# Kernel tuning notes

Hardware: AMD Instinct MI355X
Metric: run time of the kernel (lower is better)

## Reference

```python
import jax, jax.numpy as jnp
import numpy as np

D_MODEL = 1024
NUM_HEADS = 16
HEAD_DIM = D_MODEL // NUM_HEADS


def setup_inputs() -> dict:
    key = jax.random.key(0)
    kx, kq, kk, kv, ko = jax.random.split(key, 5)
    B, T = 2, 2048
    scale = 1.0 / np.sqrt(D_MODEL)
    return {
        "x": jax.random.normal(kx, (B, T, D_MODEL), dtype=jnp.float32),
        "wq": jax.random.normal(kq, (D_MODEL, D_MODEL), dtype=jnp.float32) * scale,
        "wk": jax.random.normal(kk, (D_MODEL, D_MODEL), dtype=jnp.float32) * scale,
        "wv": jax.random.normal(kv, (D_MODEL, D_MODEL), dtype=jnp.float32) * scale,
        "wo": jax.random.normal(ko, (D_MODEL, D_MODEL), dtype=jnp.float32) * scale,
    }


def _split_heads(x):
    b, t, _ = x.shape
    return x.reshape(b, t, NUM_HEADS, HEAD_DIM).transpose(0, 2, 1, 3)  # [b,h,t,d]


def reference(x, wq, wk, wv, wo):
    q = _split_heads(x @ wq)
    k = _split_heads(x @ wk)
    v = _split_heads(x @ wv)
    inv_sqrt_d = jnp.asarray(1.0 / np.sqrt(HEAD_DIM), x.dtype)
    scores = jnp.einsum("bhqd,bhkd->bhqk", q, k) * inv_sqrt_d
    weights = jax.nn.softmax(scores, axis=-1)  # dropout rate 0.0 -> identity
    out = jnp.einsum("bhqk,bhkd->bhqd", weights, v)
    b, h, t, d = out.shape
    out = out.transpose(0, 2, 1, 3).reshape(b, t, D_MODEL)
    return out @ wo
```

## Files before the change

### kernel.cpp

```cpp
#include <hip/hip_runtime.h>
#include <stdint.h>

using bf16   = __bf16;
using bf16x8 = __bf16 __attribute__((ext_vector_type(8)));
using bf16x4 = __bf16 __attribute__((ext_vector_type(4)));
using f32x4  = float  __attribute__((ext_vector_type(4)));

#define DM 1024
#define T_ 2048
#define NH 16

__device__ __forceinline__ void gl_lds16(const void* g, void* l) {
  __builtin_amdgcn_global_load_lds(
      (__attribute__((address_space(1))) void*)g,
      (__attribute__((address_space(3))) void*)l, 16, 0, 0);
}

__device__ __forceinline__ f32x4 mfma16(bf16x8 a, bf16x8 b, f32x4 c) {
  return __builtin_amdgcn_mfma_f32_16x16x32_bf16(a, b, c, 0, 0, 0);
}

__global__ __launch_bounds__(256)
void k_cast_x(const float* __restrict__ x, bf16* __restrict__ xb) {
  const size_t i = (size_t)blockIdx.x * 256 + threadIdx.x;
  const float4 a = *(const float4*)(x + i * 8);
  const float4 c = *(const float4*)(x + i * 8 + 4);
  bf16x8 v;
  v[0] = (bf16)a.x; v[1] = (bf16)a.y; v[2] = (bf16)a.z; v[3] = (bf16)a.w;
  v[4] = (bf16)c.x; v[5] = (bf16)c.y; v[6] = (bf16)c.z; v[7] = (bf16)c.w;
  *(bf16x8*)(xb + i * 8) = v;
}

__global__ __launch_bounds__(256)
void k_transpose_w4(const float* __restrict__ w0, const float* __restrict__ w1,
                    const float* __restrict__ w2, const float* __restrict__ w3,
                    bf16* __restrict__ wtq, bf16* __restrict__ wto) {
  const int z = blockIdx.z;
  const float* w = (z == 0) ? w0 : (z == 1) ? w1 : (z == 2) ? w2 : w3;
  bf16* wt = (z < 3) ? (wtq + (size_t)z * 1024 * 1024) : wto;
  const float scale = (z == 0) ? 0.125f * 1.44269504f : 1.0f;
  __shared__ float tile[64][68];
  const int tx = threadIdx.x & 15;
  const int ty = threadIdx.x >> 4;
  const int k0 = blockIdx.y * 64, n0 = blockIdx.x * 64;
#pragma unroll
  for (int j = 0; j < 4; ++j) {
    const int r = ty + 16 * j;
    const float4 v = *(const float4*)(w + (size_t)(k0 + r) * DM + n0 + tx * 4);
    tile[r][tx * 4 + 0] = v.x; tile[r][tx * 4 + 1] = v.y;
    tile[r][tx * 4 + 2] = v.z; tile[r][tx * 4 + 3] = v.w;
  }
  __syncthreads();
#pragma unroll
  for (int j = 0; j < 4; ++j) {
    const int r = ty + 16 * j;
    bf16x4 o;
    o[0] = (bf16)(tile[tx * 4 + 0][r] * scale);
    o[1] = (bf16)(tile[tx * 4 + 1][r] * scale);
    o[2] = (bf16)(tile[tx * 4 + 2][r] * scale);
    o[3] = (bf16)(tile[tx * 4 + 3][r] * scale);
    *(bf16x4*)(wt + (size_t)(n0 + r) * DM + k0 + tx * 4) = o;
  }
}

template<int MODE>
__global__ __launch_bounds__(256)
void k_gemm(const bf16* __restrict__ A, const bf16* __restrict__ BT,
            bf16* __restrict__ Qg, bf16* __restrict__ Kg, bf16* __restrict__ Vt,
            float* __restrict__ Cout) {
  constexpr int BN = (MODE == 0) ? 128 : 64;
  constexpr int NTW = BN / 32;
  __shared__ __align__(16) bf16 Ash[128 * 32];
  __shared__ __align__(16) bf16 Bsh[BN * 32];
  const int tn = blockIdx.x, tm = blockIdx.y;
  const int lane = threadIdx.x & 63, w = threadIdx.x >> 6;
  const int wm = w >> 1, wn = w & 1;
  const int r16 = lane & 15, g = lane >> 4;
  f32x4 acc[4][NTW] = {};
  const bf16* Arow = A + (size_t)tm * 128 * DM;
  const bf16* Brow = BT + (size_t)tn * BN * DM;
  for (int k0 = 0; k0 < DM; k0 += 32) {
#pragma unroll
    for (int t = 0; t < 2; ++t) {
      const int q = t * 256 + w * 64 + lane;
      gl_lds16(Arow + (size_t)(q >> 2) * DM + k0 + (q & 3) * 8, Ash + (t * 256 + w * 64) * 8);
    }
#pragma unroll
    for (int t = 0; t < BN / 64; ++t) {
      const int q = t * 256 + w * 64 + lane;
      gl_lds16(Brow + (size_t)(q >> 2) * DM + k0 + (q & 3) * 8, Bsh + (t * 256 + w * 64) * 8);
    }
    __syncthreads();
    bf16x8 af[4], bfr[NTW];
#pragma unroll
    for (int mt = 0; mt < 4; ++mt)
      af[mt] = *(const bf16x8*)(Ash + (wm * 64 + mt * 16 + r16) * 32 + g * 8);
#pragma unroll
    for (int nt = 0; nt < NTW; ++nt)
      bfr[nt] = *(const bf16x8*)(Bsh + (wn * (BN / 2) + nt * 16 + r16) * 32 + g * 8);
#pragma unroll
    for (int mt = 0; mt < 4; ++mt)
#pragma unroll
      for (int nt = 0; nt < NTW; ++nt)
        acc[mt][nt] = mfma16(af[mt], bfr[nt], acc[mt][nt]);
    __syncthreads();
  }
#pragma unroll
  for (int mt = 0; mt < 4; ++mt) {
#pragma unroll
    for (int nt = 0; nt < NTW; ++nt) {
      const int ncol = tn * BN + wn * (BN / 2) + nt * 16 + r16;
      const int m0 = tm * 128 + wm * 64 + mt * 16 + g * 4;
      if (MODE == 0) {
        const int which = ncol >> 10, nl = ncol & 1023;
        const int h = nl >> 6, d = nl & 63;
        const int b = m0 >> 11, t0 = m0 & 2047;
        if (which == 2) {
          bf16x4 pv;
#pragma unroll
          for (int r = 0; r < 4; ++r) pv[r] = (bf16)acc[mt][nt][r];
          *(bf16x4*)(Vt + ((size_t)(b * NH + h) * 64 + d) * T_ + t0) = pv;
        } else {
          bf16* dst = (which == 0) ? Qg : Kg;
#pragma unroll
          for (int r = 0; r < 4; ++r)
            dst[(((size_t)(b * NH + h) * T_ + t0 + r) << 6) + d] = (bf16)acc[mt][nt][r];
        }
      } else {
#pragma unroll
        for (int r = 0; r < 4; ++r)
          Cout[(size_t)(m0 + r) * DM + ncol] = acc[mt][nt][r];
      }
    }
  }
}

__global__ __launch_bounds__(256)
void k_attn(const bf16* __restrict__ Qg, const bf16* __restrict__ Kg,
            const bf16* __restrict__ Vtr, bf16* __restrict__ Ao) {
  __shared__ __align__(16) bf16 Ksh[2][64 * 64];
  __shared__ __align__(16) bf16 Vsh[2][64 * 64];
  __shared__ __align__(16) bf16 Psh[4][16 * 64];
  const int qt = blockIdx.x, bh = blockIdx.y;
  const int lane = threadIdx.x & 63, w = threadIdx.x >> 6;
  const int r16 = lane & 15, g = lane >> 4;
  const bf16* Qb = Qg + (size_t)bh * T_ * 64;
  const bf16* Kb = Kg + (size_t)bh * T_ * 64;
  const bf16* Vb = Vtr + (size_t)bh * 64 * T_;
  const int q0 = qt * 64 + w * 16;
  bf16x8 qb[2];
#pragma unroll
  for (int c = 0; c < 2; ++c)
    qb[c] = *(const bf16x8*)(Qb + (size_t)(q0 + r16) * 64 + c * 32 + g * 8);
  f32x4 o[4] = {};
  float llocal = 0.f;
  const int swz = (r16 & 7) << 4;
  const int srow = lane >> 3;
  const int schunk = (lane & 7) ^ srow;

  auto stage = [&](bf16* kbuf, bf16* vbuf, int kt0) {
#pragma unroll
    for (int j = 0; j < 2; ++j) {
      const int idx = w * 2 + j;
      const int row = idx * 8 + srow;
      gl_lds16(Kb + (size_t)(kt0 + row) * 64 + schunk * 8, kbuf + idx * 512);
      gl_lds16(Vb + (size_t)row * T_ + kt0 + schunk * 8, vbuf + idx * 512);
    }
  };

  stage(Ksh[0], Vsh[0], 0);
  __syncthreads();
  constexpr int NT = T_ / 64;
  for (int kt = 0; kt < NT; ++kt) {
    const int cur = kt & 1;
    if (kt + 1 < NT) stage(Ksh[cur ^ 1], Vsh[cur ^ 1], (kt + 1) * 64);
    const char* Kc = (const char*)Ksh[cur];
    const char* Vc = (const char*)Vsh[cur];
    char* Pw = (char*)Psh[w];
    f32x4 st[4] = {};
    __builtin_amdgcn_s_setprio(1);
#pragma unroll
    for (int t = 0; t < 4; ++t) {
      const int rb = (t * 16 + r16) * 128;
      const bf16x8 k0 = *(const bf16x8*)(Kc + rb + ((g * 16) ^ swz));
      const bf16x8 k1 = *(const bf16x8*)(Kc + rb + ((64 + g * 16) ^ swz));
      st[t] = mfma16(k0, qb[0], st[t]);
      st[t] = mfma16(k1, qb[1], st[t]);
    }
    __builtin_amdgcn_s_setprio(0);
#pragma unroll
    for (int t = 0; t < 4; ++t) {
      bf16x4 pk;
#pragma unroll
      for (int r = 0; r < 4; ++r) {
        const float p = __builtin_amdgcn_exp2f(st[t][r]);
        llocal += p; pk[r] = (bf16)p;
      }
      *(bf16x4*)(Pw + r16 * 128 + ((t * 32 + g * 8) ^ swz)) = pk;
    }
    asm volatile("" ::: "memory");
    __builtin_amdgcn_s_setprio(1);
#pragma unroll
    for (int c = 0; c < 2; ++c) {
      const bf16x8 pa = *(const bf16x8*)(Pw + r16 * 128 + ((c * 64 + g * 16) ^ swz));
#pragma unroll
      for (int nt = 0; nt < 4; ++nt) {
        const bf16x8 vf = *(const bf16x8*)(Vc + (nt * 16 + r16) * 128 + ((c * 64 + g * 16) ^ swz));
        o[nt] = mfma16(pa, vf, o[nt]);
      }
    }
    __builtin_amdgcn_s_setprio(0);
    __syncthreads();
  }
  llocal += __shfl_xor(llocal, 16);
  llocal += __shfl_xor(llocal, 32);
  const int b = bh >> 4, h = bh & 15;
  float linv[4];
#pragma unroll
  for (int r = 0; r < 4; ++r)
    linv[r] = 1.f / __shfl(llocal, (lane & 48) | (g * 4 + r));
#pragma unroll
  for (int nt = 0; nt < 4; ++nt)
#pragma unroll
    for (int r = 0; r < 4; ++r) {
      const int qrow = q0 + g * 4 + r;
      Ao[((size_t)(b * T_ + qrow)) * DM + h * 64 + nt * 16 + r16] =
          (bf16)(o[nt][r] * linv[r]);
    }
}

extern "C" void kernel_launch(void* const* d_in, const int* in_sizes, int n_in,
                              void* d_out, int out_size, void* d_ws, size_t ws_size,
                              hipStream_t stream) {
  const float* x  = (const float*)d_in[0];
  const float* wq = (const float*)d_in[1];
  const float* wk = (const float*)d_in[2];
  const float* wv = (const float*)d_in[3];
  const float* wo = (const float*)d_in[4];
  char* ws = (char*)d_ws;
  const size_t MB = 1024 * 1024;
  bf16* xb   = (bf16*)(ws + 0);
  bf16* wtq  = (bf16*)(ws + 8 * MB);
  bf16* wto  = (bf16*)(ws + 14 * MB);
  bf16* Qg   = (bf16*)(ws + 16 * MB);
  bf16* Kg   = (bf16*)(ws + 24 * MB);
  bf16* Vtr  = (bf16*)(ws + 32 * MB);

  k_cast_x<<<dim3(2048), dim3(256), 0, stream>>>(x, xb);
  k_transpose_w4<<<dim3(16, 16, 4), dim3(256), 0, stream>>>(wq, wk, wv, wo, wtq, wto);
  k_gemm<0><<<dim3(24, 32), dim3(256), 0, stream>>>(xb, wtq, Qg, Kg, Vtr, (float*)nullptr);
  k_attn<<<dim3(32, 32), dim3(256), 0, stream>>>(Qg, Kg, Vtr, xb);
  k_gemm<1><<<dim3(16, 32), dim3(256), 0, stream>>>(xb, wto, (bf16*)nullptr, (bf16*)nullptr,
                                                    (bf16*)nullptr, (float*)d_out);
}
```

Measured before the change: 132.5 us.

## Load K/V fragments directly from global into registers, dropping LDS staging

The attention kernel no longer stages K and V tiles into double-buffered shared memory. Each wave now loads its MFMA fragments straight from global memory into registers, relying on L2/L1 hits because the four waves of a block read the same K/V tiles. The per-iteration block barrier is replaced by an occasional s_barrier every four tiles to keep waves loosely in step, and launch bounds request 4 blocks per CU. This removes LDS traffic and synchronisation, but it quadruples global/cache load traffic and leaves little room to hide load latency within an iteration.

```diff
diff --git a/kernel.cpp b/kernel.cpp
--- a/kernel.cpp
+++ b/kernel.cpp
@@ -135,11 +135,9 @@
   }
 }
 
-__global__ __launch_bounds__(256)
+__global__ __launch_bounds__(256, 4)
 void k_attn(const bf16* __restrict__ Qg, const bf16* __restrict__ Kg,
             const bf16* __restrict__ Vtr, bf16* __restrict__ Ao) {
-  __shared__ __align__(16) bf16 Ksh[2][64 * 64];
-  __shared__ __align__(16) bf16 Vsh[2][64 * 64];
   __shared__ __align__(16) bf16 Psh[4][16 * 64];
   const int qt = blockIdx.x, bh = blockIdx.y;
   const int lane = threadIdx.x & 63, w = threadIdx.x >> 6;
@@ -155,37 +153,32 @@
   f32x4 o[4] = {};
   float llocal = 0.f;
   const int swz = (r16 & 7) << 4;
-  const int srow = lane >> 3;
-  const int schunk = (lane & 7) ^ srow;
-
-  auto stage = [&](bf16* kbuf, bf16* vbuf, int kt0) {
-#pragma unroll
-    for (int j = 0; j < 2; ++j) {
-      const int idx = w * 2 + j;
-      const int row = idx * 8 + srow;
-      gl_lds16(Kb + (size_t)(kt0 + row) * 64 + schunk * 8, kbuf + idx * 512);
-      gl_lds16(Vb + (size_t)row * T_ + kt0 + schunk * 8, vbuf + idx * 512);
-    }
-  };
-
-  stage(Ksh[0], Vsh[0], 0);
-  __syncthreads();
+  char* Pw = (char*)Psh[w];
+  const bf16* kp = Kb + (size_t)r16 * 64 + g * 8;
+  const bf16* vp = Vb + (size_t)r16 * T_ + g * 8;
+
   constexpr int NT = T_ / 64;
   for (int kt = 0; kt < NT; ++kt) {
-    const int cur = kt & 1;
-    if (kt + 1 < NT) stage(Ksh[cur ^ 1], Vsh[cur ^ 1], (kt + 1) * 64);
-    const char* Kc = (const char*)Ksh[cur];
-    const char* Vc = (const char*)Vsh[cur];
-    char* Pw = (char*)Psh[w];
+    const bf16* kq = kp + (size_t)kt * 64 * 64;
+    bf16x8 kf[4][2];
+#pragma unroll
+    for (int t = 0; t < 4; ++t)
+#pragma unroll
+      for (int c = 0; c < 2; ++c)
+        kf[t][c] = *(const bf16x8*)(kq + t * 16 * 64 + c * 32);
+    const bf16* vq = vp + kt * 64;
+    bf16x8 vf[2][4];
+#pragma unroll
+    for (int c = 0; c < 2; ++c)
+#pragma unroll
+      for (int nt = 0; nt < 4; ++nt)
+        vf[c][nt] = *(const bf16x8*)(vq + (size_t)nt * 16 * T_ + c * 32);
     f32x4 st[4] = {};
     __builtin_amdgcn_s_setprio(1);
 #pragma unroll
     for (int t = 0; t < 4; ++t) {
-      const int rb = (t * 16 + r16) * 128;
-      const bf16x8 k0 = *(const bf16x8*)(Kc + rb + ((g * 16) ^ swz));
-      const bf16x8 k1 = *(const bf16x8*)(Kc + rb + ((64 + g * 16) ^ swz));
-      st[t] = mfma16(k0, qb[0], st[t]);
-      st[t] = mfma16(k1, qb[1], st[t]);
+      st[t] = mfma16(kf[t][0], qb[0], st[t]);
+      st[t] = mfma16(kf[t][1], qb[1], st[t]);
     }
     __builtin_amdgcn_s_setprio(0);
 #pragma unroll
@@ -204,13 +197,11 @@
     for (int c = 0; c < 2; ++c) {
       const bf16x8 pa = *(const bf16x8*)(Pw + r16 * 128 + ((c * 64 + g * 16) ^ swz));
 #pragma unroll
-      for (int nt = 0; nt < 4; ++nt) {
-        const bf16x8 vf = *(const bf16x8*)(Vc + (nt * 16 + r16) * 128 + ((c * 64 + g * 16) ^ swz));
-        o[nt] = mfma16(pa, vf, o[nt]);
-      }
+      for (int nt = 0; nt < 4; ++nt)
+        o[nt] = mfma16(pa, vf[c][nt], o[nt]);
     }
     __builtin_amdgcn_s_setprio(0);
-    __syncthreads();
+    if ((kt & 3) == 3) __builtin_amdgcn_s_barrier();
   }
   llocal += __shfl_xor(llocal, 16);
   llocal += __shfl_xor(llocal, 32);
```

Result: slower. 297.5 us (+124.6%).
